# Kernel optimization log

Hardware: AMD Instinct MI355X
Metric: run time of the kernel (lower is better)

## Reference

```python
import jax, jax.numpy as jnp
import numpy as np

N_NODES = 50000
N_EDGES = 500000
D_IN = 128
D_HID = 128
OUTPUT_DIM = 10.0


def gcn_conv(x, src, dst, edge_weight, W, b, n_nodes):
    # PyG GCNConv: out = D^{-1/2} (A + I) D^{-1/2} X W + b, self-loop weight 1
    xw = x @ W  # [N, D_out]
    # degree at target nodes, including self-loop weight 1
    deg = jax.ops.segment_sum(edge_weight, dst, num_segments=n_nodes) + 1.0
    dinv = jnp.where(deg > 0, jax.lax.rsqrt(deg), 0.0)  # [N]
    norm = dinv[src] * edge_weight * dinv[dst]  # [E]
    msgs = xw[src] * norm[:, None]  # [E, D_out] gathered+scaled messages
    agg = jax.ops.segment_sum(msgs, dst, num_segments=n_nodes)
    # analytic self-loop contribution: norm_ii = dinv_i * 1 * dinv_i
    agg = agg + xw * (dinv * dinv)[:, None]
    return agg + b


def setup_inputs() -> dict:
    key = jax.random.key(0)
    k = jax.random.split(key, 8)
    x = jax.random.normal(k[0], (N_NODES, D_IN), dtype=jnp.float32)
    edge_index = jax.random.randint(k[1], (2, N_EDGES), 0, N_NODES, dtype=jnp.int64)
    edge_weight = jax.random.uniform(k[2], (N_EDGES,), dtype=jnp.float32)
    s1 = 1.0 / np.sqrt(D_IN)
    s2 = 1.0 / np.sqrt(D_HID)
    W1 = jax.random.uniform(k[3], (D_IN, D_HID), minval=-s1, maxval=s1, dtype=jnp.float32)
    b1 = jnp.zeros((D_HID,), dtype=jnp.float32)
    W2 = jax.random.uniform(k[4], (D_HID, D_HID), minval=-s2, maxval=s2, dtype=jnp.float32)
    b2 = jnp.zeros((D_HID,), dtype=jnp.float32)
    Wf = jax.random.uniform(k[5], (D_HID, 1), minval=-s2, maxval=s2, dtype=jnp.float32)
    bf = jax.random.uniform(k[6], (1,), minval=-s2, maxval=s2, dtype=jnp.float32)
    return {"x": x, "edge_index": edge_index, "edge_weight": edge_weight,
            "W1": W1, "b1": b1, "W2": W2, "b2": b2, "Wf": Wf, "bf": bf}


def reference(x, edge_index, edge_weight, W1, b1, W2, b2, Wf, bf):
    src, dst = edge_index[0], edge_index[1]
    h = gcn_conv(x, src, dst, edge_weight, W1, b1, N_NODES)
    h = gcn_conv(h, src, dst, edge_weight, W2, b2, N_NODES)
    out = h @ Wf + bf  # [N, 1]
    return jax.nn.sigmoid(out) * OUTPUT_DIM
```

## Files before the change

### kernel.cpp

```cpp
#include <hip/hip_runtime.h>

#define N_NODES 50000
#define N_EDGES 500000
#define D 128
#define FXS 4194304.0f
#define CAP 64
#define DPAD 8
#define EBLK 489
#define GEMVB 2048

typedef unsigned long long u64;

__global__ void prep_kernel(const float* __restrict__ W1, const float* __restrict__ W2,
                            const float* __restrict__ b1, const float* __restrict__ b2,
                            const float* __restrict__ Wf, const float* __restrict__ bf,
                            float* __restrict__ v, float* __restrict__ consts,
                            u64* __restrict__ degcnt) {
    const int t = threadIdx.x;
    if (blockIdx.x == 0) {
        __shared__ float u[D];
        if (t < D) {
            float a = 0.f;
#pragma unroll 8
            for (int j = 0; j < D; ++j) a += W2[t * D + j] * Wf[j];
            u[t] = a;
        }
        __syncthreads();
        if (t < D) {
            float a = 0.f;
#pragma unroll 8
            for (int k = 0; k < D; ++k) a += W1[t * D + k] * u[k];
            v[t] = a;
        }
        if (t == 0) {
            float c = 0.f;
            for (int k = 0; k < D; ++k) c += b1[k] * u[k];
            consts[0] = c;
        } else if (t == 1) {
            float c = bf[0];
            for (int k = 0; k < D; ++k) c += b2[k] * Wf[k];
            consts[1] = c;
        }
        return;
    }
    for (int i = (blockIdx.x - 1) * 256 + t; i < N_NODES * DPAD; i += 255 * 256)
        degcnt[i] = 0ull;
}

__global__ void work_kernel(const int* __restrict__ src, const int* __restrict__ dst,
                            const float* __restrict__ ew, const float* __restrict__ x,
                            const float* __restrict__ v,
                            u64* __restrict__ degcnt, int2* __restrict__ pairs,
                            float* __restrict__ traw) {
    const int t = threadIdx.x;
    const int bid = blockIdx.x;
    if (bid < EBLK) {
        int q = bid * 256 + t;
        if (q < N_EDGES / 4) {
            int4   d4 = ((const int4*)dst)[q];
            int4   s4 = ((const int4*)src)[q];
            float4 w4 = ((const float4*)ew)[q];
            unsigned f0 = __float2uint_rn(w4.x * FXS);
            unsigned f1 = __float2uint_rn(w4.y * FXS);
            unsigned f2 = __float2uint_rn(w4.z * FXS);
            unsigned f3 = __float2uint_rn(w4.w * FXS);
            u64 o0 = atomicAdd(&degcnt[(size_t)d4.x * DPAD], (1ull << 32) | (u64)f0);
            u64 o1 = atomicAdd(&degcnt[(size_t)d4.y * DPAD], (1ull << 32) | (u64)f1);
            u64 o2 = atomicAdd(&degcnt[(size_t)d4.z * DPAD], (1ull << 32) | (u64)f2);
            u64 o3 = atomicAdd(&degcnt[(size_t)d4.w * DPAD], (1ull << 32) | (u64)f3);
            int s0 = (int)(o0 >> 32), s1 = (int)(o1 >> 32);
            int s2 = (int)(o2 >> 32), s3 = (int)(o3 >> 32);
            if (s0 < CAP) pairs[(size_t)d4.x * CAP + s0] = make_int2(s4.x, __float_as_int(w4.x));
            if (s1 < CAP) pairs[(size_t)d4.y * CAP + s1] = make_int2(s4.y, __float_as_int(w4.y));
            if (s2 < CAP) pairs[(size_t)d4.z * CAP + s2] = make_int2(s4.z, __float_as_int(w4.z));
            if (s3 < CAP) pairs[(size_t)d4.w * CAP + s3] = make_int2(s4.w, __float_as_int(w4.w));
        }
        return;
    }
    __shared__ float vs[D];
    if (t < D) vs[t] = v[t];
    __syncthreads();
    const int l = t & 31;
    const int sub = t >> 5;
    for (int g = bid - EBLK; g < N_NODES / 8; g += GEMVB) {
        int n = g * 8 + sub;
        float4 xv = ((const float4*)(x + (size_t)n * D))[l];
        float a = xv.x * vs[l * 4] + xv.y * vs[l * 4 + 1] +
                  xv.z * vs[l * 4 + 2] + xv.w * vs[l * 4 + 3];
#pragma unroll
        for (int off = 16; off > 0; off >>= 1) a += __shfl_xor(a, off);
        if (l == 0) traw[n] = a;
    }
}

__global__ void epi_kernel(const u64* __restrict__ degcnt, const float* __restrict__ traw,
                           float* __restrict__ dinv, int* __restrict__ cntv,
                           float* __restrict__ tw) {
    int n = blockIdx.x * blockDim.x + threadIdx.x;
    if (n < N_NODES) {
        u64 dc = degcnt[(size_t)n * DPAD];
        int c = (int)(dc >> 32);
        float deg = (float)(unsigned)(dc & 0xffffffffu) * (1.0f / FXS);
        float di = rsqrtf(deg + 1.0f);
        dinv[n] = di;
        cntv[n] = (c < CAP) ? c : CAP;
        tw[n] = di * traw[n];
    }
}

__global__ void gather_s_kernel(const float* __restrict__ tw, const float* __restrict__ dinv,
                                const int* __restrict__ cntv, const int2* __restrict__ pairs,
                                const float* __restrict__ consts, float* __restrict__ sw) {
    int tid = threadIdx.x;
    int n = blockIdx.x * 64 + (tid >> 2);
    int l = tid & 3;
    if (n >= N_NODES) return;
    int cnt = cntv[n];
    const int4* row = (const int4*)(pairs + (size_t)n * CAP);
    float acc = 0.f;
    for (int c = l; 2 * c < cnt; c += 4) {
        int4 p = row[c];
        acc += __int_as_float(p.y) * tw[p.x];
        if (2 * c + 1 < cnt) acc += __int_as_float(p.w) * tw[p.z];
    }
    acc += __shfl_xor(acc, 1);
    acc += __shfl_xor(acc, 2);
    if (l == 0) {
        float di = dinv[n];
        float s = di * (acc + tw[n]) + consts[0];
        sw[n] = di * s;
    }
}

__global__ void gather_z_kernel(const float* __restrict__ sw, const float* __restrict__ dinv,
                                const int* __restrict__ cntv, const int2* __restrict__ pairs,
                                const float* __restrict__ consts, float* __restrict__ out) {
    int tid = threadIdx.x;
    int n = blockIdx.x * 64 + (tid >> 2);
    int l = tid & 3;
    if (n >= N_NODES) return;
    int cnt = cntv[n];
    const int4* row = (const int4*)(pairs + (size_t)n * CAP);
    float acc = 0.f;
    for (int c = l; 2 * c < cnt; c += 4) {
        int4 p = row[c];
        acc += __int_as_float(p.y) * sw[p.x];
        if (2 * c + 1 < cnt) acc += __int_as_float(p.w) * sw[p.z];
    }
    acc += __shfl_xor(acc, 1);
    acc += __shfl_xor(acc, 2);
    if (l == 0) {
        float di = dinv[n];
        float z = di * (acc + sw[n]) + consts[1];
        out[n] = 10.0f / (1.0f + expf(-z));
    }
}

extern "C" void kernel_launch(void* const* d_in, const int* in_sizes, int n_in,
                              void* d_out, int out_size, void* d_ws, size_t ws_size,
                              hipStream_t stream) {
    const float* x  = (const float*)d_in[0];
    const int*   ei = (const int*)d_in[1];
    const float* ew = (const float*)d_in[2];
    const float* W1 = (const float*)d_in[3];
    const float* b1 = (const float*)d_in[4];
    const float* W2 = (const float*)d_in[5];
    const float* b2 = (const float*)d_in[6];
    const float* Wf = (const float*)d_in[7];
    const float* bf = (const float*)d_in[8];
    const int* srcv = ei;
    const int* dstv = ei + N_EDGES;
    float* out = (float*)d_out;

    char* p = (char*)d_ws;
    auto alloc = [&](size_t bytes) { void* r = (void*)p; p += (bytes + 255) & ~(size_t)255; return r; };
    u64*   degcnt = (u64*)alloc((size_t)N_NODES * DPAD * 8);
    float* dinv   = (float*)alloc(N_NODES * 4);
    int*   cntv   = (int*)alloc(N_NODES * 4);
    float* traw   = (float*)alloc(N_NODES * 4);
    float* tw     = (float*)alloc(N_NODES * 4);
    float* sw     = (float*)alloc(N_NODES * 4);
    float* v      = (float*)alloc(D * 4);
    float* consts = (float*)alloc(2 * 4);
    int2*  pairs  = (int2*)alloc((size_t)N_NODES * CAP * 8);

    const int GB = (N_NODES + 63) / 64;
    const int NB = (N_NODES + 255) / 256;

    prep_kernel<<<256, 256, 0, stream>>>(W1, W2, b1, b2, Wf, bf, v, consts, degcnt);

    work_kernel<<<EBLK + GEMVB, 256, 0, stream>>>(srcv, dstv, ew, x, v,
                                                  degcnt, pairs, traw);

    epi_kernel<<<NB, 256, 0, stream>>>(degcnt, traw, dinv, cntv, tw);

    gather_s_kernel<<<GB, 256, 0, stream>>>(tw, dinv, cntv, pairs, consts, sw);
    gather_z_kernel<<<GB, 256, 0, stream>>>(sw, dinv, cntv, pairs, consts, out);
}
```

Baseline: 139.0 us.

## Fuse all stages into one persistent kernel with grid barriers

Replaces the five kernel launches with a single persistent kernel of 512 blocks that separates phases with atomic-counter grid barriers. Each block recomputes the small weight-folding GEMV into shared memory, so the prep stage and its global round trip go away. The degree counters are no longer padded (DPAD removed), and counters plus barrier are cleared with a memset. This removes launch gaps and inter-kernel drains, but adds barrier spin cost and redundant per-block weight reads, and unpadded counters may contend more under atomics.

```diff
diff --git a/kernel.cpp b/kernel.cpp
--- a/kernel.cpp
+++ b/kernel.cpp
@@ -5,100 +5,101 @@
 #define D 128
 #define FXS 4194304.0f
 #define CAP 64
-#define DPAD 8
-#define EBLK 489
-#define GEMVB 2048
+#define GRID 512
+#define NT 256
+#define TOT (GRID * NT)
+#define NQ (N_EDGES / 4)
 
 typedef unsigned long long u64;
 
-__global__ void prep_kernel(const float* __restrict__ W1, const float* __restrict__ W2,
-                            const float* __restrict__ b1, const float* __restrict__ b2,
-                            const float* __restrict__ Wf, const float* __restrict__ bf,
-                            float* __restrict__ v, float* __restrict__ consts,
-                            u64* __restrict__ degcnt) {
-    const int t = threadIdx.x;
-    if (blockIdx.x == 0) {
-        __shared__ float u[D];
-        if (t < D) {
-            float a = 0.f;
-#pragma unroll 8
-            for (int j = 0; j < D; ++j) a += W2[t * D + j] * Wf[j];
-            u[t] = a;
-        }
-        __syncthreads();
-        if (t < D) {
-            float a = 0.f;
-#pragma unroll 8
-            for (int k = 0; k < D; ++k) a += W1[t * D + k] * u[k];
-            v[t] = a;
-        }
-        if (t == 0) {
-            float c = 0.f;
-            for (int k = 0; k < D; ++k) c += b1[k] * u[k];
-            consts[0] = c;
-        } else if (t == 1) {
-            float c = bf[0];
-            for (int k = 0; k < D; ++k) c += b2[k] * Wf[k];
-            consts[1] = c;
-        }
-        return;
+__device__ __forceinline__ void gbar(unsigned* bar, unsigned target) {
+    __syncthreads();
+    if (threadIdx.x == 0) {
+        __hip_atomic_fetch_add(bar, 1u, __ATOMIC_ACQ_REL, __HIP_MEMORY_SCOPE_AGENT);
+        while (__hip_atomic_load(bar, __ATOMIC_ACQUIRE, __HIP_MEMORY_SCOPE_AGENT) < target)
+            __builtin_amdgcn_s_sleep(8);
     }
-    for (int i = (blockIdx.x - 1) * 256 + t; i < N_NODES * DPAD; i += 255 * 256)
-        degcnt[i] = 0ull;
+    __syncthreads();
 }
 
-__global__ void work_kernel(const int* __restrict__ src, const int* __restrict__ dst,
-                            const float* __restrict__ ew, const float* __restrict__ x,
-                            const float* __restrict__ v,
-                            u64* __restrict__ degcnt, int2* __restrict__ pairs,
-                            float* __restrict__ traw) {
+__global__ __launch_bounds__(NT, 2) void fused_kernel(
+    const int* __restrict__ src, const int* __restrict__ dst, const float* __restrict__ ew,
+    const float* __restrict__ x,
+    const float* __restrict__ W1, const float* __restrict__ W2,
+    const float* __restrict__ b1, const float* __restrict__ b2,
+    const float* __restrict__ Wf, const float* __restrict__ bf,
+    u64* __restrict__ degcnt, int2* __restrict__ pairs,
+    float* __restrict__ traw, float* __restrict__ dinv, int* __restrict__ cntv,
+    float* __restrict__ tw, float* __restrict__ sw, float* __restrict__ out,
+    unsigned* __restrict__ bar) {
     const int t = threadIdx.x;
     const int bid = blockIdx.x;
-    if (bid < EBLK) {
-        int q = bid * 256 + t;
-        if (q < N_EDGES / 4) {
-            int4   d4 = ((const int4*)dst)[q];
-            int4   s4 = ((const int4*)src)[q];
-            float4 w4 = ((const float4*)ew)[q];
-            unsigned f0 = __float2uint_rn(w4.x * FXS);
-            unsigned f1 = __float2uint_rn(w4.y * FXS);
-            unsigned f2 = __float2uint_rn(w4.z * FXS);
-            unsigned f3 = __float2uint_rn(w4.w * FXS);
-            u64 o0 = atomicAdd(&degcnt[(size_t)d4.x * DPAD], (1ull << 32) | (u64)f0);
-            u64 o1 = atomicAdd(&degcnt[(size_t)d4.y * DPAD], (1ull << 32) | (u64)f1);
-            u64 o2 = atomicAdd(&degcnt[(size_t)d4.z * DPAD], (1ull << 32) | (u64)f2);
-            u64 o3 = atomicAdd(&degcnt[(size_t)d4.w * DPAD], (1ull << 32) | (u64)f3);
-            int s0 = (int)(o0 >> 32), s1 = (int)(o1 >> 32);
-            int s2 = (int)(o2 >> 32), s3 = (int)(o3 >> 32);
-            if (s0 < CAP) pairs[(size_t)d4.x * CAP + s0] = make_int2(s4.x, __float_as_int(w4.x));
-            if (s1 < CAP) pairs[(size_t)d4.y * CAP + s1] = make_int2(s4.y, __float_as_int(w4.y));
-            if (s2 < CAP) pairs[(size_t)d4.z * CAP + s2] = make_int2(s4.z, __float_as_int(w4.z));
-            if (s3 < CAP) pairs[(size_t)d4.w * CAP + s3] = make_int2(s4.w, __float_as_int(w4.w));
+    const int gtid = bid * NT + t;
+    __shared__ float ush[D];
+    __shared__ float vsh[D];
+    __shared__ float csh[2];
+
+    if (t < D) {
+        float a = 0.f;
+#pragma unroll 8
+        for (int j = 0; j < D; ++j) a += W2[t * D + j] * Wf[j];
+        ush[t] = a;
+    }
+    __syncthreads();
+    if (t < D) {
+        float a = 0.f;
+#pragma unroll 8
+        for (int k = 0; k < D; ++k) a += W1[t * D + k] * ush[k];
+        vsh[t] = a;
+    }
+    if (t == 0) {
+        float c = 0.f;
+        for (int k = 0; k < D; ++k) c += b1[k] * ush[k];
+        csh[0] = c;
+    } else if (t == 1) {
+        float c = bf[0];
+        for (int k = 0; k < D; ++k) c += b2[k] * Wf[k];
+        csh[1] = c;
+    }
+    __syncthreads();
+
+    for (int q = gtid; q < NQ; q += TOT) {
+        int4   d4 = ((const int4*)dst)[q];
+        int4   s4 = ((const int4*)src)[q];
+        float4 w4 = ((const float4*)ew)[q];
+        unsigned f0 = __float2uint_rn(w4.x * FXS);
+        unsigned f1 = __float2uint_rn(w4.y * FXS);
+        unsigned f2 = __float2uint_rn(w4.z * FXS);
+        unsigned f3 = __float2uint_rn(w4.w * FXS);
+        u64 o0 = atomicAdd(&degcnt[d4.x], (1ull << 32) | (u64)f0);
+        u64 o1 = atomicAdd(&degcnt[d4.y], (1ull << 32) | (u64)f1);
+        u64 o2 = atomicAdd(&degcnt[d4.z], (1ull << 32) | (u64)f2);
+        u64 o3 = atomicAdd(&degcnt[d4.w], (1ull << 32) | (u64)f3);
+        int s0 = (int)(o0 >> 32), s1 = (int)(o1 >> 32);
+        int s2 = (int)(o2 >> 32), s3 = (int)(o3 >> 32);
+        if (s0 < CAP) pairs[(size_t)d4.x * CAP + s0] = make_int2(s4.x, __float_as_int(w4.x));
+        if (s1 < CAP) pairs[(size_t)d4.y * CAP + s1] = make_int2(s4.y, __float_as_int(w4.y));
+        if (s2 < CAP) pairs[(size_t)d4.z * CAP + s2] = make_int2(s4.z, __float_as_int(w4.z));
+        if (s3 < CAP) pairs[(size_t)d4.w * CAP + s3] = make_int2(s4.w, __float_as_int(w4.w));
+    }
+
+    {
+        const int l = t & 31;
+        const int sub = t >> 5;
+        for (int g = bid; g < N_NODES / 8; g += GRID) {
+            int n = g * 8 + sub;
+            float4 xv = ((const float4*)(x + (size_t)n * D))[l];
+            float a = xv.x * vsh[l * 4] + xv.y * vsh[l * 4 + 1] +
+                      xv.z * vsh[l * 4 + 2] + xv.w * vsh[l * 4 + 3];
+#pragma unroll
+            for (int off = 16; off > 0; off >>= 1) a += __shfl_xor(a, off);
+            if (l == 0) traw[n] = a;
         }
-        return;
     }
-    __shared__ float vs[D];
-    if (t < D) vs[t] = v[t];
-    __syncthreads();
-    const int l = t & 31;
-    const int sub = t >> 5;
-    for (int g = bid - EBLK; g < N_NODES / 8; g += GEMVB) {
-        int n = g * 8 + sub;
-        float4 xv = ((const float4*)(x + (size_t)n * D))[l];
-        float a = xv.x * vs[l * 4] + xv.y * vs[l * 4 + 1] +
-                  xv.z * vs[l * 4 + 2] + xv.w * vs[l * 4 + 3];
-#pragma unroll
-        for (int off = 16; off > 0; off >>= 1) a += __shfl_xor(a, off);
-        if (l == 0) traw[n] = a;
-    }
-}
+    gbar(bar, 1 * GRID);
 
-__global__ void epi_kernel(const u64* __restrict__ degcnt, const float* __restrict__ traw,
-                           float* __restrict__ dinv, int* __restrict__ cntv,
-                           float* __restrict__ tw) {
-    int n = blockIdx.x * blockDim.x + threadIdx.x;
-    if (n < N_NODES) {
-        u64 dc = degcnt[(size_t)n * DPAD];
+    for (int n = gtid; n < N_NODES; n += TOT) {
+        u64 dc = degcnt[n];
         int c = (int)(dc >> 32);
         float deg = (float)(unsigned)(dc & 0xffffffffu) * (1.0f / FXS);
         float di = rsqrtf(deg + 1.0f);
@@ -106,53 +107,56 @@
         cntv[n] = (c < CAP) ? c : CAP;
         tw[n] = di * traw[n];
     }
-}
+    gbar(bar, 2 * GRID);
 
-__global__ void gather_s_kernel(const float* __restrict__ tw, const float* __restrict__ dinv,
-                                const int* __restrict__ cntv, const int2* __restrict__ pairs,
-                                const float* __restrict__ consts, float* __restrict__ sw) {
-    int tid = threadIdx.x;
-    int n = blockIdx.x * 64 + (tid >> 2);
-    int l = tid & 3;
-    if (n >= N_NODES) return;
-    int cnt = cntv[n];
-    const int4* row = (const int4*)(pairs + (size_t)n * CAP);
-    float acc = 0.f;
-    for (int c = l; 2 * c < cnt; c += 4) {
-        int4 p = row[c];
-        acc += __int_as_float(p.y) * tw[p.x];
-        if (2 * c + 1 < cnt) acc += __int_as_float(p.w) * tw[p.z];
+    {
+        const int l = t & 3;
+        const int sub = t >> 2;
+        for (int g = bid; g < (N_NODES + 63) / 64; g += GRID) {
+            int n = g * 64 + sub;
+            if (n < N_NODES) {
+                int cnt = cntv[n];
+                const int4* row = (const int4*)(pairs + (size_t)n * CAP);
+                float acc = 0.f;
+                for (int c = l; 2 * c < cnt; c += 4) {
+                    int4 pr = row[c];
+                    acc += __int_as_float(pr.y) * tw[pr.x];
+                    if (2 * c + 1 < cnt) acc += __int_as_float(pr.w) * tw[pr.z];
+                }
+                acc += __shfl_xor(acc, 1);
+                acc += __shfl_xor(acc, 2);
+                if (l == 0) {
+                    float di = dinv[n];
+                    sw[n] = di * (di * (acc + tw[n]) + csh[0]);
+                }
+            }
+        }
     }
-    acc += __shfl_xor(acc, 1);
-    acc += __shfl_xor(acc, 2);
-    if (l == 0) {
-        float di = dinv[n];
-        float s = di * (acc + tw[n]) + consts[0];
-        sw[n] = di * s;
-    }
-}
+    gbar(bar, 3 * GRID);
 
-__global__ void gather_z_kernel(const float* __restrict__ sw, const float* __restrict__ dinv,
-                                const int* __restrict__ cntv, const int2* __restrict__ pairs,
-                                const float* __restrict__ consts, float* __restrict__ out) {
-    int tid = threadIdx.x;
-    int n = blockIdx.x * 64 + (tid >> 2);
-    int l = tid & 3;
-    if (n >= N_NODES) return;
-    int cnt = cntv[n];
-    const int4* row = (const int4*)(pairs + (size_t)n * CAP);
-    float acc = 0.f;
-    for (int c = l; 2 * c < cnt; c += 4) {
-        int4 p = row[c];
-        acc += __int_as_float(p.y) * sw[p.x];
-        if (2 * c + 1 < cnt) acc += __int_as_float(p.w) * sw[p.z];
-    }
-    acc += __shfl_xor(acc, 1);
-    acc += __shfl_xor(acc, 2);
-    if (l == 0) {
-        float di = dinv[n];
-        float z = di * (acc + sw[n]) + consts[1];
-        out[n] = 10.0f / (1.0f + expf(-z));
+    {
+        const int l = t & 3;
+        const int sub = t >> 2;
+        for (int g = bid; g < (N_NODES + 63) / 64; g += GRID) {
+            int n = g * 64 + sub;
+            if (n < N_NODES) {
+                int cnt = cntv[n];
+                const int4* row = (const int4*)(pairs + (size_t)n * CAP);
+                float acc = 0.f;
+                for (int c = l; 2 * c < cnt; c += 4) {
+                    int4 pr = row[c];
+                    acc += __int_as_float(pr.y) * sw[pr.x];
+                    if (2 * c + 1 < cnt) acc += __int_as_float(pr.w) * sw[pr.z];
+                }
+                acc += __shfl_xor(acc, 1);
+                acc += __shfl_xor(acc, 2);
+                if (l == 0) {
+                    float di = dinv[n];
+                    float z = di * (acc + sw[n]) + csh[1];
+                    out[n] = 10.0f / (1.0f + expf(-z));
+                }
+            }
+        }
     }
 }
 
@@ -174,26 +178,20 @@
 
     char* p = (char*)d_ws;
     auto alloc = [&](size_t bytes) { void* r = (void*)p; p += (bytes + 255) & ~(size_t)255; return r; };
-    u64*   degcnt = (u64*)alloc((size_t)N_NODES * DPAD * 8);
+    char* zbase = p;
+    unsigned* bar    = (unsigned*)alloc(256);
+    u64*      degcnt = (u64*)alloc((size_t)N_NODES * 8);
+    size_t zbytes = (size_t)(p - zbase);
+    float* traw   = (float*)alloc(N_NODES * 4);
     float* dinv   = (float*)alloc(N_NODES * 4);
     int*   cntv   = (int*)alloc(N_NODES * 4);
-    float* traw   = (float*)alloc(N_NODES * 4);
     float* tw     = (float*)alloc(N_NODES * 4);
     float* sw     = (float*)alloc(N_NODES * 4);
-    float* v      = (float*)alloc(D * 4);
-    float* consts = (float*)alloc(2 * 4);
     int2*  pairs  = (int2*)alloc((size_t)N_NODES * CAP * 8);
 
-    const int GB = (N_NODES + 63) / 64;
-    const int NB = (N_NODES + 255) / 256;
+    hipMemsetAsync(zbase, 0, zbytes, stream);
 
-    prep_kernel<<<256, 256, 0, stream>>>(W1, W2, b1, b2, Wf, bf, v, consts, degcnt);
-
-    work_kernel<<<EBLK + GEMVB, 256, 0, stream>>>(srcv, dstv, ew, x, v,
-                                                  degcnt, pairs, traw);
-
-    epi_kernel<<<NB, 256, 0, stream>>>(degcnt, traw, dinv, cntv, tw);
-
-    gather_s_kernel<<<GB, 256, 0, stream>>>(tw, dinv, cntv, pairs, consts, sw);
-    gather_z_kernel<<<GB, 256, 0, stream>>>(sw, dinv, cntv, pairs, consts, out);
+    fused_kernel<<<GRID, NT, 0, stream>>>(srcv, dstv, ew, x, W1, W2, b1, b2, Wf, bf,
+                                          degcnt, pairs, traw, dinv, cntv, tw, sw, out,
+                                          bar);
 }
```

Measured after the change: 292.5 us. 110% more time.
